# Performance work log

Hardware: AMD Instinct MI355X
Metric: run time of the kernel (lower is better)

## Reference

```python
import jax, jax.numpy as jnp
import numpy as np
from jax import lax

RADIUS = (5, 5, 5)
EPS = 1e-5


def _box_sum(x, radius=RADIUS):
    # Separable all-ones box filter == F.conv3d(x, ones((1,1,)+radius), padding='same')
    # x: [N, 1, D, H, W]
    dn = lax.conv_dimension_numbers(x.shape, (1, 1) + radius, ('NCDHW', 'OIDHW', 'NCDHW'))
    for axis, k in zip((2, 3, 4), radius):
        kshape = [1, 1, 1, 1, 1]
        kshape[axis] = k
        kern = jnp.ones(kshape, dtype=x.dtype)
        dn_ax = lax.conv_dimension_numbers(x.shape, tuple(kshape), ('NCDHW', 'OIDHW', 'NCDHW'))
        x = lax.conv_general_dilated(x, kern, window_strides=(1, 1, 1), padding='SAME',
                                     dimension_numbers=dn_ax)
    return x


def _image_gradient(img):
    # torch.gradient over spatial dims (central diff interior, one-sided edges)
    g = jnp.gradient(img, axis=(2, 3, 4))
    return jnp.concatenate(g, axis=1)  # [N, 3, D, H, W]


def setup_inputs() -> dict:
    key = jax.random.key(0)
    k1, k2, k3, k4 = jax.random.split(key, 4)
    shape = (1, 1, 192, 192, 192)
    moving_image = jax.random.normal(k1, shape, dtype=jnp.float32)
    fixed_image = jax.random.normal(k2, shape, dtype=jnp.float32)
    moving_mask = jax.random.randint(k3, shape, 0, 2).astype(jnp.bool_)
    fixed_mask = jax.random.randint(k4, shape, 0, 2).astype(jnp.bool_)
    original_image_spacing = jnp.ones((3,), dtype=jnp.int32)
    return {
        'moving_image': moving_image,
        'fixed_image': fixed_image,
        'moving_mask': moving_mask,
        'fixed_mask': fixed_mask,
        'original_image_spacing': original_image_spacing,
    }


def reference(moving_image, fixed_image, moving_mask, fixed_mask, original_image_spacing):
    npix = float(np.prod(RADIUS))  # 125

    # dual method: union mask applied to both gradients, total grad halved
    union = jnp.logical_or(moving_mask, fixed_mask).astype(moving_image.dtype)
    grad_moving = _image_gradient(moving_image) * union
    grad_fixed = _image_gradient(fixed_image) * union
    total_grad = (grad_moving + grad_fixed) * 0.5

    sum_m = _box_sum(moving_image)
    sum_f = _box_sum(fixed_image)
    sum_mm = _box_sum(moving_image * moving_image)
    sum_ff = _box_sum(fixed_image * fixed_image)
    sum_mf = _box_sum(moving_image * fixed_image)

    moving_mean = sum_m / npix
    fixed_mean = sum_f / npix

    var_m = sum_mm - 2 * moving_mean * sum_m + npix * moving_mean * moving_mean
    var_f = sum_ff - 2 * fixed_mean * sum_f + npix * fixed_mean * fixed_mean
    var_mf = var_m * var_f
    cross = sum_mf - fixed_mean * sum_m - moving_mean * sum_f + npix * moving_mean * fixed_mean

    moving_mean_centered = moving_image - moving_mean
    fixed_mean_centered = fixed_image - fixed_mean

    mask = (var_mf > EPS) & (var_f > EPS) & (fixed_mean_centered != 0.0) & (moving_mean_centered != 0.0)
    var_mf_safe = jnp.where(mask, var_mf, 1.0)
    var_f_safe = jnp.where(mask, var_f, 1.0)
    factor = jnp.where(
        mask,
        2.0 * cross / var_mf_safe * (moving_mean_centered - cross * fixed_mean_centered / var_f_safe),
        0.0,
    )

    return -1.0 * factor * total_grad
```

## Files before the change

### kernel.cpp

```cpp
#include <hip/hip_runtime.h>


#define DD 192
#define HH 192
#define WW 192
#define NVOX (DD * HH * WW)
#define SLICE (HH * WW)
#define TS 16
#define RR 20
#define RW 24
#define ZSEG 12
#define NBX 12
#define NBY 12
#define NBZ 16
#define NBLK (NBX * NBY * NBZ)
#define PER_XCD (NBLK / 8)

__global__ __launch_bounds__(256)
void ncc_forces_kernel(const float* __restrict__ mimg,
                       const float* __restrict__ fimg,
                       const int*   __restrict__ mmask,
                       const int*   __restrict__ fmask,
                       float* __restrict__ out)
{
    __shared__ float rawm[RR][RW];
    __shared__ float rawf[RR][RW];
    __shared__ float xs[5][RR][20];
    __shared__ float Tf[4][RR][20];
    __shared__ float box[2][TS][5][20];

    const int b  = blockIdx.x;
    const int L  = (b & 7) * PER_XCD + (b >> 3);
    const int bz = L / (NBX * NBY);
    const int r_ = L - bz * (NBX * NBY);
    const int by = r_ / NBX;
    const int bx = r_ - by * NBX;

    const int tid = threadIdx.x;
    const int tx = tid & 15, ty = tid >> 4;
    const int x0 = bx * TS, y0 = by * TS, z0 = bz * ZSEG;

    const int  simg   = tid / 120;
    const bool stager = (simg < 2);
    const int  st     = tid - simg * 120;
    const int  srow   = st / 6;
    const int  squad  = st - srow * 6;
    const int  sgy    = y0 - 2 + srow;
    const int  sgx    = x0 - 4 + 4 * squad;
    const bool sin_   = (sgy >= 0) && (sgy < HH) && (sgx >= 0) && (sgx <= WW - 4);
    const float* sptr = (simg == 1) ? fimg : mimg;
    float* sldsb = (simg == 1) ? &rawf[0][0] : &rawm[0][0];
    const int  sloff  = srow * RW + 4 * squad;

    float4 pref = make_float4(0, 0, 0, 0);
    auto prefetch = [&](int zz) {
        pref = make_float4(0, 0, 0, 0);
        if (stager && sin_ && zz >= 0 && zz < DD)
            pref = *(const float4*)(sptr + ((size_t)zz * HH + sgy) * WW + sgx);
    };

    float ring[5][5];
#pragma unroll
    for (int s = 0; s < 5; ++s)
#pragma unroll
        for (int f = 0; f < 5; ++f) ring[s][f] = 0.f;
    float cm[5] = {0, 0, 0, 0, 0}, cf[5] = {0, 0, 0, 0, 0};

    const int gx = x0 + tx, gy = y0 + ty;
    const int vbase = (z0 * HH + gy) * WW + gx;
    int umN = 0, ufN = 0;

    prefetch(z0 - 2);

    for (int n = 0; n <= ZSEG + 4; ++n) {
        const int zc = z0 - 2 + n;
        const int z  = zc - 3;
        const bool emitv = (n >= 5);

        if (stager) *(float4*)(sldsb + sloff) = pref;
        prefetch(zc + 1);

        const int um = umN, uf = ufN;
        if (n >= 4 && n < ZSEG + 4) {
            const int vn = vbase + (n - 4) * SLICE;
            umN = __builtin_nontemporal_load(mmask + vn);
            ufN = __builtin_nontemporal_load(fmask + vn);
        }

        __syncthreads();

        if (tid < 80) {
            const int yy = tid >> 2;
            const int t4 = (tid & 3) * 4;
            const float4 A0 = *(const float4*)&rawm[yy][t4];
            const float4 A1 = *(const float4*)&rawm[yy][t4 + 4];
            const float2 A2 = *(const float2*)&rawm[yy][t4 + 8];
            const float4 B0 = *(const float4*)&rawf[yy][t4];
            const float4 B1 = *(const float4*)&rawf[yy][t4 + 4];
            const float2 B2 = *(const float2*)&rawf[yy][t4 + 8];
            const float a[10]  = {A0.x, A0.y, A0.z, A0.w, A1.x, A1.y, A1.z, A1.w, A2.x, A2.y};
            const float bb[10] = {B0.x, B0.y, B0.z, B0.w, B1.x, B1.y, B1.z, B1.w, B2.x, B2.y};
            float p[10], s, w0, w1, w2, w3;
#pragma unroll
            for (int f = 0; f < 5; ++f) {
#pragma unroll
                for (int i = 2; i < 10; ++i) {
                    p[i] = (f == 0) ? a[i] : (f == 1) ? bb[i] :
                           (f == 2) ? a[i] * a[i] : (f == 3) ? bb[i] * bb[i] : a[i] * bb[i];
                }
                s = p[2] + p[3] + p[4] + p[5] + p[6]; w0 = s;
                s += p[7] - p[2]; w1 = s;
                s += p[8] - p[3]; w2 = s;
                s += p[9] - p[4]; w3 = s;
                *(float4*)&xs[f][yy][t4] = make_float4(w0, w1, w2, w3);
            }
            const int tw = n & 3;
            *(float4*)&Tf[tw][yy][t4] =
                make_float4(a[2] + bb[2], a[3] + bb[3], a[4] + bb[4], a[5] + bb[5]);
            if (t4 == 12)
                *(float4*)&Tf[tw][yy][16] =
                    make_float4(a[6] + bb[6], a[7] + bb[7], a[8] + bb[8], a[9] + bb[9]);
        }

        {
            const float ncm = rawm[ty + 2][tx + 4];
            const float ncf = rawf[ty + 2][tx + 4];
#pragma unroll
            for (int s2 = 4; s2 > 0; --s2) { cm[s2] = cm[s2 - 1]; cf[s2] = cf[s2 - 1]; }
            cm[0] = ncm; cf[0] = ncf;
        }
        if (n >= 1) {
            const int pp = (n - 1) & 1;
            const float* bq = &box[pp][tx][0][ty];
            const float s0 = bq[0], s1 = bq[20], s2v = bq[40], s3 = bq[60], s4 = bq[80];
#pragma unroll
            for (int s = 0; s < 4; ++s)
#pragma unroll
                for (int f = 0; f < 5; ++f) ring[s][f] = ring[s + 1][f];
            ring[4][0] = s0; ring[4][1] = s1; ring[4][2] = s2v; ring[4][3] = s3; ring[4][4] = s4;
        }

        if (emitv) {
            float sum_m = 0.f, sum_f = 0.f, sum_mm = 0.f, sum_ff = 0.f, sum_mf = 0.f;
#pragma unroll
            for (int s = 0; s < 5; ++s) {
                sum_m  += ring[s][0];
                sum_f  += ring[s][1];
                sum_mm += ring[s][2];
                sum_ff += ring[s][3];
                sum_mf += ring[s][4];
            }
            const int vidx = vbase + (n - 5) * SLICE;
            const int tsl = (n + 1) & 3;
            const int cy = ty + 2;
            const float mc = cm[3];
            const float fc = cf[3];
            const float Tc = mc + fc;

            const float* tp = &Tf[tsl][cy][tx + 1];
            const float Txm = tp[0], Txp = tp[2];
            const float* tq = &Tf[tsl][cy - 1][tx + 2];
            const float Tym = tq[0], Typ = tq[40];

            float gsx, gsy, gsz;
            if (gx == 0)          gsx = Txp - Tc;
            else if (gx == WW-1)  gsx = Tc - Txm;
            else                  gsx = 0.5f * (Txp - Txm);
            if (gy == 0)          gsy = Typ - Tc;
            else if (gy == HH-1)  gsy = Tc - Tym;
            else                  gsy = 0.5f * (Typ - Tym);
            const float Tzm = cm[4] + cf[4], Tzp = cm[2] + cf[2];
            if (z == 0)           gsz = Tzp - Tc;
            else if (z == DD-1)   gsz = Tc - Tzm;
            else                  gsz = 0.5f * (Tzp - Tzm);

            const float u = ((um != 0) || (uf != 0)) ? 1.0f : 0.0f;

            const float npix = 125.0f;
            const float inv_npix = 1.0f / 125.0f;
            const float mean_m = sum_m * inv_npix;
            const float mean_f = sum_f * inv_npix;
            const float var_m = sum_mm - 2.0f * mean_m * sum_m + npix * mean_m * mean_m;
            const float var_f = sum_ff - 2.0f * mean_f * sum_f + npix * mean_f * mean_f;
            const float var_mf = var_m * var_f;
            const float cross = sum_mf - mean_f * sum_m - mean_m * sum_f + npix * mean_m * mean_f;
            const float mmc = mc - mean_m;
            const float fmc = fc - mean_f;
            const bool ok = (var_mf > 1e-5f) && (var_f > 1e-5f) && (fmc != 0.0f) && (mmc != 0.0f);
            float factor = 0.0f;
            if (ok) factor = 2.0f * cross / var_mf * (mmc - cross * fmc / var_f);

            const float nf = -factor * 0.5f * u;
            out[vidx]            = nf * gsz;
            out[NVOX + vidx]     = nf * gsy;
            out[2 * NVOX + vidx] = nf * gsx;
        }

        __syncthreads();

        if (tid < 160) {
            const int x  = tid & 15;
            const int c8 = ((tid >> 4) & 1) * 8;
            const int f  = tid >> 5;
            const float* xp = &xs[f][c8][x];
            float v[12];
#pragma unroll
            for (int j = 0; j < 12; ++j) v[j] = xp[20 * j];
            float o[8];
            float s = v[0] + v[1] + v[2] + v[3] + v[4];
            o[0] = s;
#pragma unroll
            for (int j = 1; j < 8; ++j) { s += v[j + 4] - v[j - 1]; o[j] = s; }
            float* bp = &box[n & 1][x][f][c8];
            *(float4*)bp       = make_float4(o[0], o[1], o[2], o[3]);
            *(float4*)(bp + 4) = make_float4(o[4], o[5], o[6], o[7]);
        }
    }
}

extern "C" void kernel_launch(void* const* d_in, const int* in_sizes, int n_in,
                              void* d_out, int out_size, void* d_ws, size_t ws_size,
                              hipStream_t stream)
{
    const float* mimg  = (const float*)d_in[0];
    const float* fimg  = (const float*)d_in[1];
    const int*   mmask = (const int*)d_in[2];
    const int*   fmask = (const int*)d_in[3];
    float* out = (float*)d_out;

    dim3 grid(NBLK, 1, 1);
    dim3 block(256, 1, 1);
    hipLaunchKernelGGL(ncc_forces_kernel, grid, block, 0, stream,
                       mimg, fimg, mmask, fmask, out);
}
```

Baseline: 210.3 us.

## Restructure to single-wavefront 16x4 tiles with register ring and direct gradients

Replaces the 256-thread 16x16 tile with a 64-thread (one wavefront) 16x4 tile spanning 16 z-slices. Each block now has 6912 blocks in a 12x48x12 grid. The y-box sum is computed directly per thread from a small shared buffer, and the z-box ring buffer is indexed by a fully unrolled 5-slice loop. This removes the Tf/box shared staging and makes every thread do all stages, so barriers only cover one wavefront. In exchange the y-halo overhead rises sharply: 8 rows are loaded for 4 output rows, which adds redundant global reads and x-pass work.

```diff
diff --git a/kernel.cpp b/kernel.cpp
--- a/kernel.cpp
+++ b/kernel.cpp
@@ -6,28 +6,27 @@
 #define WW 192
 #define NVOX (DD * HH * WW)
 #define SLICE (HH * WW)
-#define TS 16
-#define RR 20
-#define RW 24
-#define ZSEG 12
+#define TSX 16
+#define TSY 4
+#define SR 8
+#define SC 24
+#define ZSEG 16
 #define NBX 12
-#define NBY 12
-#define NBZ 16
+#define NBY 48
+#define NBZ 12
 #define NBLK (NBX * NBY * NBZ)
 #define PER_XCD (NBLK / 8)
 
-__global__ __launch_bounds__(256)
+__global__ __launch_bounds__(64, 4)
 void ncc_forces_kernel(const float* __restrict__ mimg,
                        const float* __restrict__ fimg,
                        const int*   __restrict__ mmask,
                        const int*   __restrict__ fmask,
                        float* __restrict__ out)
 {
-    __shared__ float rawm[RR][RW];
-    __shared__ float rawf[RR][RW];
-    __shared__ float xs[5][RR][20];
-    __shared__ float Tf[4][RR][20];
-    __shared__ float box[2][TS][5][20];
+    __shared__ float rawm[SR][SC];
+    __shared__ float rawf[SR][SC];
+    __shared__ float xs[5][SR][TSX];
 
     const int b  = blockIdx.x;
     const int L  = (b & 7) * PER_XCD + (b >> 3);
@@ -36,184 +35,160 @@
     const int by = r_ / NBX;
     const int bx = r_ - by * NBX;
 
-    const int tid = threadIdx.x;
-    const int tx = tid & 15, ty = tid >> 4;
-    const int x0 = bx * TS, y0 = by * TS, z0 = bz * ZSEG;
-
-    const int  simg   = tid / 120;
-    const bool stager = (simg < 2);
-    const int  st     = tid - simg * 120;
-    const int  srow   = st / 6;
-    const int  squad  = st - srow * 6;
-    const int  sgy    = y0 - 2 + srow;
-    const int  sgx    = x0 - 4 + 4 * squad;
-    const bool sin_   = (sgy >= 0) && (sgy < HH) && (sgx >= 0) && (sgx <= WW - 4);
-    const float* sptr = (simg == 1) ? fimg : mimg;
-    float* sldsb = (simg == 1) ? &rawf[0][0] : &rawm[0][0];
-    const int  sloff  = srow * RW + 4 * squad;
-
-    float4 pref = make_float4(0, 0, 0, 0);
-    auto prefetch = [&](int zz) {
-        pref = make_float4(0, 0, 0, 0);
-        if (stager && sin_ && zz >= 0 && zz < DD)
-            pref = *(const float4*)(sptr + ((size_t)zz * HH + sgy) * WW + sgx);
+    const int lane = threadIdx.x;
+    const int tx = lane & 15, ty = lane >> 4;
+    const int xr = lane >> 3, xo = lane & 7;
+    const int x0 = bx * TSX, y0 = by * TSY, z0 = bz * ZSEG;
+
+    const int  q1    = (lane < 48) ? lane : (lane - 48);
+    const bool img1f = (lane >= 48);
+    const int  r1q   = q1 / 6, c1q = (q1 - r1q * 6) * 4;
+    const int  q2    = 16 + lane;
+    const int  r2q   = q2 / 6, c2q = (q2 - r2q * 6) * 4;
+    const int  sgy1  = y0 - 2 + r1q, sgx1 = x0 - 4 + c1q;
+    const int  sgy2  = y0 - 2 + r2q, sgx2 = x0 - 4 + c2q;
+    const bool in1   = (sgy1 >= 0) && (sgy1 < HH) && (sgx1 >= 0) && (sgx1 <= WW - 4);
+    const bool in2   = (lane < 32) && (sgy2 >= 0) && (sgy2 < HH) && (sgx2 >= 0) && (sgx2 <= WW - 4);
+    const float* sp1 = img1f ? fimg : mimg;
+    float* sd1 = img1f ? &rawf[0][0] : &rawm[0][0];
+    const int so1 = r1q * SC + c1q;
+    const int so2 = r2q * SC + c2q;
+
+    float4 A = make_float4(0, 0, 0, 0), Bv = make_float4(0, 0, 0, 0);
+    auto prefetch = [&](int zz, bool en) {
+        A = make_float4(0, 0, 0, 0); Bv = make_float4(0, 0, 0, 0);
+        if (en && zz >= 0 && zz < DD) {
+            if (in1) A  = *(const float4*)(sp1  + ((size_t)zz * HH + sgy1) * WW + sgx1);
+            if (in2) Bv = *(const float4*)(fimg + ((size_t)zz * HH + sgy2) * WW + sgx2);
+        }
     };
 
     float ring[5][5];
 #pragma unroll
-    for (int s = 0; s < 5; ++s)
-#pragma unroll
-        for (int f = 0; f < 5; ++f) ring[s][f] = 0.f;
-    float cm[5] = {0, 0, 0, 0, 0}, cf[5] = {0, 0, 0, 0, 0};
+    for (int sl = 0; sl < 5; ++sl)
+#pragma unroll
+        for (int f = 0; f < 5; ++f) ring[sl][f] = 0.f;
+    float cm[4] = {0, 0, 0, 0}, cf[4] = {0, 0, 0, 0};
+    float gsxr[3] = {0, 0, 0}, gsyr[3] = {0, 0, 0};
+    int umC = 0, ufC = 0, umN = 0, ufN = 0;
 
     const int gx = x0 + tx, gy = y0 + ty;
-    const int vbase = (z0 * HH + gy) * WW + gx;
-    int umN = 0, ufN = 0;
-
-    prefetch(z0 - 2);
-
-    for (int n = 0; n <= ZSEG + 4; ++n) {
-        const int zc = z0 - 2 + n;
-        const int z  = zc - 3;
-        const bool emitv = (n >= 5);
-
-        if (stager) *(float4*)(sldsb + sloff) = pref;
-        prefetch(zc + 1);
-
-        const int um = umN, uf = ufN;
-        if (n >= 4 && n < ZSEG + 4) {
-            const int vn = vbase + (n - 4) * SLICE;
-            umN = __builtin_nontemporal_load(mmask + vn);
-            ufN = __builtin_nontemporal_load(fmask + vn);
-        }
-
-        __syncthreads();
-
-        if (tid < 80) {
-            const int yy = tid >> 2;
-            const int t4 = (tid & 3) * 4;
-            const float4 A0 = *(const float4*)&rawm[yy][t4];
-            const float4 A1 = *(const float4*)&rawm[yy][t4 + 4];
-            const float2 A2 = *(const float2*)&rawm[yy][t4 + 8];
-            const float4 B0 = *(const float4*)&rawf[yy][t4];
-            const float4 B1 = *(const float4*)&rawf[yy][t4 + 4];
-            const float2 B2 = *(const float2*)&rawf[yy][t4 + 8];
-            const float a[10]  = {A0.x, A0.y, A0.z, A0.w, A1.x, A1.y, A1.z, A1.w, A2.x, A2.y};
-            const float bb[10] = {B0.x, B0.y, B0.z, B0.w, B1.x, B1.y, B1.z, B1.w, B2.x, B2.y};
-            float p[10], s, w0, w1, w2, w3;
-#pragma unroll
-            for (int f = 0; f < 5; ++f) {
-#pragma unroll
-                for (int i = 2; i < 10; ++i) {
-                    p[i] = (f == 0) ? a[i] : (f == 1) ? bb[i] :
-                           (f == 2) ? a[i] * a[i] : (f == 3) ? bb[i] * bb[i] : a[i] * bb[i];
+
+    prefetch(z0 - 2, true);
+
+    for (int no = 0; no < 4; ++no) {
+#pragma unroll
+        for (int ni = 0; ni < 5; ++ni) {
+            const int n = no * 5 + ni;
+            const int s = z0 - 2 + n;
+
+            *(float4*)(sd1 + so1) = A;
+            if (lane < 32) *(float4*)(&rawf[0][0] + so2) = Bv;
+            prefetch(s + 1, n < ZSEG + 3);
+
+            umC = umN; ufC = ufN;
+            if (n >= 3 && n <= ZSEG + 2) {
+                const size_t vq = ((size_t)(z0 - 3 + n) * HH + gy) * WW + gx;
+                umN = __builtin_nontemporal_load(mmask + vq);
+                ufN = __builtin_nontemporal_load(fmask + vq);
+            }
+
+            __syncthreads();
+
+            {
+                const float ncm = rawm[ty + 2][tx + 4];
+                const float ncf = rawf[ty + 2][tx + 4];
+                const float Txm = rawm[ty + 2][tx + 3] + rawf[ty + 2][tx + 3];
+                const float Txp = rawm[ty + 2][tx + 5] + rawf[ty + 2][tx + 5];
+                const float Tym = rawm[ty + 1][tx + 4] + rawf[ty + 1][tx + 4];
+                const float Typ = rawm[ty + 3][tx + 4] + rawf[ty + 3][tx + 4];
+                const float Tc  = ncm + ncf;
+                const float ngsx = (gx == 0) ? (Txp - Tc) :
+                                   (gx == WW - 1) ? (Tc - Txm) : 0.5f * (Txp - Txm);
+                const float ngsy = (gy == 0) ? (Typ - Tc) :
+                                   (gy == HH - 1) ? (Tc - Tym) : 0.5f * (Typ - Tym);
+                gsxr[2] = gsxr[1]; gsxr[1] = gsxr[0]; gsxr[0] = ngsx;
+                gsyr[2] = gsyr[1]; gsyr[1] = gsyr[0]; gsyr[0] = ngsy;
+                cm[3] = cm[2]; cm[2] = cm[1]; cm[1] = cm[0]; cm[0] = ncm;
+                cf[3] = cf[2]; cf[2] = cf[1]; cf[1] = cf[0]; cf[0] = ncf;
+            }
+
+            {
+                const float2 M0 = *(const float2*)&rawm[xr][2 * xo + 2];
+                const float2 M1 = *(const float2*)&rawm[xr][2 * xo + 4];
+                const float2 M2 = *(const float2*)&rawm[xr][2 * xo + 6];
+                const float2 F0 = *(const float2*)&rawf[xr][2 * xo + 2];
+                const float2 F1 = *(const float2*)&rawf[xr][2 * xo + 4];
+                const float2 F2 = *(const float2*)&rawf[xr][2 * xo + 6];
+                const float m6[6] = {M0.x, M0.y, M1.x, M1.y, M2.x, M2.y};
+                const float f6[6] = {F0.x, F0.y, F1.x, F1.y, F2.x, F2.y};
+#pragma unroll
+                for (int f = 0; f < 5; ++f) {
+                    float v[6];
+#pragma unroll
+                    for (int i = 0; i < 6; ++i)
+                        v[i] = (f == 0) ? m6[i] : (f == 1) ? f6[i] :
+                               (f == 2) ? m6[i] * m6[i] : (f == 3) ? f6[i] * f6[i]
+                                        : m6[i] * f6[i];
+                    const float X0 = v[0] + v[1] + v[2] + v[3] + v[4];
+                    const float X1 = X0 + v[5] - v[0];
+                    *(float2*)&xs[f][xr][2 * xo] = make_float2(X0, X1);
                 }
-                s = p[2] + p[3] + p[4] + p[5] + p[6]; w0 = s;
-                s += p[7] - p[2]; w1 = s;
-                s += p[8] - p[3]; w2 = s;
-                s += p[9] - p[4]; w3 = s;
-                *(float4*)&xs[f][yy][t4] = make_float4(w0, w1, w2, w3);
-            }
-            const int tw = n & 3;
-            *(float4*)&Tf[tw][yy][t4] =
-                make_float4(a[2] + bb[2], a[3] + bb[3], a[4] + bb[4], a[5] + bb[5]);
-            if (t4 == 12)
-                *(float4*)&Tf[tw][yy][16] =
-                    make_float4(a[6] + bb[6], a[7] + bb[7], a[8] + bb[8], a[9] + bb[9]);
-        }
-
-        {
-            const float ncm = rawm[ty + 2][tx + 4];
-            const float ncf = rawf[ty + 2][tx + 4];
-#pragma unroll
-            for (int s2 = 4; s2 > 0; --s2) { cm[s2] = cm[s2 - 1]; cf[s2] = cf[s2 - 1]; }
-            cm[0] = ncm; cf[0] = ncf;
-        }
-        if (n >= 1) {
-            const int pp = (n - 1) & 1;
-            const float* bq = &box[pp][tx][0][ty];
-            const float s0 = bq[0], s1 = bq[20], s2v = bq[40], s3 = bq[60], s4 = bq[80];
-#pragma unroll
-            for (int s = 0; s < 4; ++s)
-#pragma unroll
-                for (int f = 0; f < 5; ++f) ring[s][f] = ring[s + 1][f];
-            ring[4][0] = s0; ring[4][1] = s1; ring[4][2] = s2v; ring[4][3] = s3; ring[4][4] = s4;
-        }
-
-        if (emitv) {
-            float sum_m = 0.f, sum_f = 0.f, sum_mm = 0.f, sum_ff = 0.f, sum_mf = 0.f;
-#pragma unroll
-            for (int s = 0; s < 5; ++s) {
-                sum_m  += ring[s][0];
-                sum_f  += ring[s][1];
-                sum_mm += ring[s][2];
-                sum_ff += ring[s][3];
-                sum_mf += ring[s][4];
-            }
-            const int vidx = vbase + (n - 5) * SLICE;
-            const int tsl = (n + 1) & 3;
-            const int cy = ty + 2;
-            const float mc = cm[3];
-            const float fc = cf[3];
-            const float Tc = mc + fc;
-
-            const float* tp = &Tf[tsl][cy][tx + 1];
-            const float Txm = tp[0], Txp = tp[2];
-            const float* tq = &Tf[tsl][cy - 1][tx + 2];
-            const float Tym = tq[0], Typ = tq[40];
-
-            float gsx, gsy, gsz;
-            if (gx == 0)          gsx = Txp - Tc;
-            else if (gx == WW-1)  gsx = Tc - Txm;
-            else                  gsx = 0.5f * (Txp - Txm);
-            if (gy == 0)          gsy = Typ - Tc;
-            else if (gy == HH-1)  gsy = Tc - Tym;
-            else                  gsy = 0.5f * (Typ - Tym);
-            const float Tzm = cm[4] + cf[4], Tzp = cm[2] + cf[2];
-            if (z == 0)           gsz = Tzp - Tc;
-            else if (z == DD-1)   gsz = Tc - Tzm;
-            else                  gsz = 0.5f * (Tzp - Tzm);
-
-            const float u = ((um != 0) || (uf != 0)) ? 1.0f : 0.0f;
-
-            const float npix = 125.0f;
-            const float inv_npix = 1.0f / 125.0f;
-            const float mean_m = sum_m * inv_npix;
-            const float mean_f = sum_f * inv_npix;
-            const float var_m = sum_mm - 2.0f * mean_m * sum_m + npix * mean_m * mean_m;
-            const float var_f = sum_ff - 2.0f * mean_f * sum_f + npix * mean_f * mean_f;
-            const float var_mf = var_m * var_f;
-            const float cross = sum_mf - mean_f * sum_m - mean_m * sum_f + npix * mean_m * mean_f;
-            const float mmc = mc - mean_m;
-            const float fmc = fc - mean_f;
-            const bool ok = (var_mf > 1e-5f) && (var_f > 1e-5f) && (fmc != 0.0f) && (mmc != 0.0f);
-            float factor = 0.0f;
-            if (ok) factor = 2.0f * cross / var_mf * (mmc - cross * fmc / var_f);
-
-            const float nf = -factor * 0.5f * u;
-            out[vidx]            = nf * gsz;
-            out[NVOX + vidx]     = nf * gsy;
-            out[2 * NVOX + vidx] = nf * gsx;
-        }
-
-        __syncthreads();
-
-        if (tid < 160) {
-            const int x  = tid & 15;
-            const int c8 = ((tid >> 4) & 1) * 8;
-            const int f  = tid >> 5;
-            const float* xp = &xs[f][c8][x];
-            float v[12];
-#pragma unroll
-            for (int j = 0; j < 12; ++j) v[j] = xp[20 * j];
-            float o[8];
-            float s = v[0] + v[1] + v[2] + v[3] + v[4];
-            o[0] = s;
-#pragma unroll
-            for (int j = 1; j < 8; ++j) { s += v[j + 4] - v[j - 1]; o[j] = s; }
-            float* bp = &box[n & 1][x][f][c8];
-            *(float4*)bp       = make_float4(o[0], o[1], o[2], o[3]);
-            *(float4*)(bp + 4) = make_float4(o[4], o[5], o[6], o[7]);
+            }
+
+            __syncthreads();
+
+#pragma unroll
+            for (int f = 0; f < 5; ++f)
+                ring[ni][f] = xs[f][ty][tx] + xs[f][ty + 1][tx] + xs[f][ty + 2][tx]
+                            + xs[f][ty + 3][tx] + xs[f][ty + 4][tx];
+
+            if (n >= 4) {
+                float sum_m = 0.f, sum_f = 0.f, sum_mm = 0.f, sum_ff = 0.f, sum_mf = 0.f;
+#pragma unroll
+                for (int sl = 0; sl < 5; ++sl) {
+                    sum_m  += ring[sl][0];
+                    sum_f  += ring[sl][1];
+                    sum_mm += ring[sl][2];
+                    sum_ff += ring[sl][3];
+                    sum_mf += ring[sl][4];
+                }
+                const int z = z0 - 4 + n;
+                const size_t vidx = ((size_t)z * HH + gy) * WW + gx;
+                const float mc = cm[2];
+                const float fc = cf[2];
+                const float Tc = mc + fc;
+                const float Tzp = cm[1] + cf[1];
+                const float Tzm = cm[3] + cf[3];
+                float gsz;
+                if (z == 0)           gsz = Tzp - Tc;
+                else if (z == DD - 1) gsz = Tc - Tzm;
+                else                  gsz = 0.5f * (Tzp - Tzm);
+                const float gsx = gsxr[2], gsy = gsyr[2];
+
+                const float u = ((umC != 0) || (ufC != 0)) ? 1.0f : 0.0f;
+
+                const float npix = 125.0f;
+                const float inv_npix = 1.0f / 125.0f;
+                const float mean_m = sum_m * inv_npix;
+                const float mean_f = sum_f * inv_npix;
+                const float var_m = sum_mm - 2.0f * mean_m * sum_m + npix * mean_m * mean_m;
+                const float var_f = sum_ff - 2.0f * mean_f * sum_f + npix * mean_f * mean_f;
+                const float var_mf = var_m * var_f;
+                const float cross = sum_mf - mean_f * sum_m - mean_m * sum_f
+                                  + npix * mean_m * mean_f;
+                const float mmc = mc - mean_m;
+                const float fmc = fc - mean_f;
+                const bool ok = (var_mf > 1e-5f) && (var_f > 1e-5f) &&
+                                (fmc != 0.0f) && (mmc != 0.0f);
+                float factor = 0.0f;
+                if (ok) factor = 2.0f * cross / var_mf * (mmc - cross * fmc / var_f);
+
+                const float nf = -factor * 0.5f * u;
+                out[vidx]            = nf * gsz;
+                out[NVOX + vidx]     = nf * gsy;
+                out[2 * NVOX + vidx] = nf * gsx;
+            }
         }
     }
 }
@@ -229,7 +204,7 @@
     float* out = (float*)d_out;
 
     dim3 grid(NBLK, 1, 1);
-    dim3 block(256, 1, 1);
+    dim3 block(64, 1, 1);
     hipLaunchKernelGGL(ncc_forces_kernel, grid, block, 0, stream,
                        mimg, fimg, mmask, fmask, out);
 }
```

New measurement: 218.7 us. 1.04x slower.
